# Optimization experiments

Hardware: AMD Instinct MI355X
Metric: run time of the kernel (lower is better)

The kernel has to match this reference:

```python
import jax, jax.numpy as jnp
import numpy as np

V, E, H, DH, C, B, T = 50000, 256, 256, 512, 5, 64, 2048


def setup_inputs() -> dict:
    key = jax.random.key(0)
    ks = jax.random.split(key, 10)
    s = lambda k, sh: (jax.random.normal(k, sh, jnp.float32) * 0.05)
    seqs = jax.random.randint(ks[0], (B, T), 0, V)
    # descending sorted lengths, max length == T (matches max_len = sorted_lens[0])
    lens = jnp.sort(jax.random.randint(ks[1], (B,), T // 4, T + 1))[::-1]
    lens = lens.at[0].set(T).astype(jnp.int32)
    return {
        "seqs": seqs, "lens": lens,
        "emb": s(ks[2], (V, E)),
        "W_ih_f": s(ks[3], (3 * H, E)), "W_hh_f": s(ks[4], (3 * H, H)),
        "b_ih_f": jnp.zeros(3 * H, jnp.float32), "b_hh_f": jnp.zeros(3 * H, jnp.float32),
        "W_ih_b": s(ks[5], (3 * H, E)), "W_hh_b": s(ks[6], (3 * H, H)),
        "b_ih_b": jnp.zeros(3 * H, jnp.float32), "b_hh_b": jnp.zeros(3 * H, jnp.float32),
        "W1": s(ks[7], (DH, 2 * H)), "b1": jnp.zeros(DH, jnp.float32),
        "W2": s(ks[8], (C, DH)), "b2": jnp.zeros(C, jnp.float32),
    }


def _gru_scan(xs, W_ih, W_hh, b_ih, b_hh):
    """xs: [T,B,E]; torch GRUCell semantics, gate order r,z,n. Returns final h [B,H]."""
    gi = jnp.einsum('tbe,ge->tbg', xs, W_ih) + b_ih  # input projections, all steps

    def step(h, gi_t):
        gh = h @ W_hh.T + b_hh
        ir, iz, i_n = jnp.split(gi_t, 3, axis=-1)
        hr, hz, hn = jnp.split(gh, 3, axis=-1)
        r = jax.nn.sigmoid(ir + hr)
        z = jax.nn.sigmoid(iz + hz)
        n = jnp.tanh(i_n + r * hn)
        return (1.0 - z) * n + z * h, None

    h0 = jnp.zeros((xs.shape[1], W_hh.shape[1]), xs.dtype)
    hT, _ = jax.lax.scan(step, h0, gi)
    return hT


def reference(seqs, lens, emb, W_ih_f, W_hh_f, b_ih_f, b_hh_f,
              W_ih_b, W_hh_b, b_ih_b, b_hh_b, W1, b1, W2, b2):
    x = emb[seqs]  # [B,T,E]
    # original LEFT-pads embedded sequences with zeros to max_len
    valid = (jnp.arange(T)[None, :] >= (T - lens)[:, None]).astype(x.dtype)  # [B,T]
    x = x * valid[:, :, None]
    xs = jnp.swapaxes(x, 0, 1)  # [T,B,E]
    hf = _gru_scan(xs, W_ih_f, W_hh_f, b_ih_f, b_hh_f)
    hb = _gru_scan(xs[::-1], W_ih_b, W_hh_b, b_ih_b, b_hh_b)
    rep = jnp.concatenate([hf, hb], axis=1)  # [B,2H]
    h1 = jax.nn.relu(rep @ W1.T + b1)  # dropout is identity in eval
    return jax.nn.softmax(h1 @ W2.T + b2, axis=-1)
```

## Files before the change

### kernel.cpp

```cpp
#include <hip/hip_runtime.h>
#include <stdint.h>

typedef uint32_t u32; typedef uint16_t u16;
typedef __attribute__((ext_vector_type(8))) __bf16 bf16x8;
typedef __attribute__((ext_vector_type(4))) float f32x4;
typedef __attribute__((ext_vector_type(2))) u32 u32x2;
typedef __attribute__((ext_vector_type(4))) u32 u32x4;

#define Vv 50000
#define Ee 256
#define Hh 256
#define Gg 768
#define Bb 64
#define Tt 2048

__device__ __forceinline__ u16 f2bf(float f) {
  u32 x = __builtin_bit_cast(u32, f);
  return (u16)((x + 0x7FFFu + ((x >> 16) & 1u)) >> 16);
}
__device__ __forceinline__ float bf2f(u16 b) {
  u32 x = ((u32)b) << 16;
  return __builtin_bit_cast(float, x);
}
__device__ __forceinline__ u32 pack2(float a, float b) {
  return (u32)f2bf(a) | ((u32)f2bf(b) << 16);
}
__device__ __forceinline__ float sigm(float x) {
  float e = __builtin_amdgcn_exp2f(-1.44269504089f * x);
  return __builtin_amdgcn_rcpf(1.0f + e);
}
__device__ __forceinline__ float tanh_fast(float x) {
  float e = __builtin_amdgcn_exp2f(2.88539008178f * x);
  return 1.0f - 2.0f * __builtin_amdgcn_rcpf(e + 1.0f);
}
__device__ __forceinline__ float bfx(u32x2 v, int q) {
  u32 word = (q & 2) ? v[1] : v[0];
  u16 h = (q & 1) ? (u16)(word >> 16) : (u16)(word & 0xffffu);
  return bf2f(h);
}
__device__ __forceinline__ void block_sync_lds() {
  asm volatile("s_waitcnt lgkmcnt(0)" ::: "memory");
  __builtin_amdgcn_s_barrier();
  asm volatile("" ::: "memory");
}

__global__ void k0_bias(const float* __restrict__ bih_f, const float* __restrict__ bhh_f,
                        const float* __restrict__ bih_b, const float* __restrict__ bhh_b,
                        u16* __restrict__ Pf, u16* __restrict__ Pb) {
  int c = threadIdx.x + blockIdx.x * 256;
  if (c < Gg) {
    float bf_ = bih_f[c] + (c < 512 ? bhh_f[c] : 0.f);
    float bb_ = bih_b[c] + (c < 512 ? bhh_b[c] : 0.f);
    Pf[(size_t)Vv * Gg + c] = f2bf(bf_);
    Pb[(size_t)Vv * Gg + c] = f2bf(bb_);
  }
}

__global__ __launch_bounds__(256) void k1_proj(
    const float* __restrict__ emb, const float* __restrict__ Wih_f,
    const float* __restrict__ Wih_b,
    const float* __restrict__ bih_f, const float* __restrict__ bhh_f,
    const float* __restrict__ bih_b, const float* __restrict__ bhh_b,
    u16* __restrict__ Pf, u16* __restrict__ Pb)
{
  const int t = threadIdx.x, w = t >> 6, l = t & 63;
  const int cl = l & 15, rq = l >> 4;
  const int m0 = blockIdx.x * 128;
  const int dir = blockIdx.y;
  const float* Wih = dir ? Wih_b : Wih_f;
  const float* bih = dir ? bih_b : bih_f;
  const float* bhh = dir ? bhh_b : bhh_f;
  u16* Pd = dir ? Pb : Pf;

  __shared__ __align__(16) u16 As[4096 * 8];
  __shared__ __align__(16) u16 Bs[2048 * 8];

  for (int i = t; i < 4096; i += 256) {
    const int kt = i >> 9, rem = i & 511, row = rem >> 2, rqv = rem & 3;
    const int gm = m0 + row;
    float4 a0 = {0.f,0.f,0.f,0.f}, a1 = {0.f,0.f,0.f,0.f};
    if (gm < Vv) {
      const float* src = emb + (size_t)gm * Ee + kt * 32 + rqv * 8;
      a0 = *(const float4*)src;
      a1 = *(const float4*)(src + 4);
    }
    u32x4 uv = { pack2(a0.x, a0.y), pack2(a0.z, a0.w),
                 pack2(a1.x, a1.y), pack2(a1.z, a1.w) };
    *(u32x4*)(As + (size_t)i * 8) = uv;
  }
  __syncthreads();

  for (int nb = 0; nb < 12; ++nb) {
    for (int i = t; i < 2048; i += 256) {
      const int kt = i >> 8, rem = i & 255, r2 = rem >> 2, rqv = rem & 3;
      const float* src = Wih + (size_t)(nb * 64 + r2) * Ee + kt * 32 + rqv * 8;
      const float4 b0 = *(const float4*)src;
      const float4 b1 = *(const float4*)(src + 4);
      u32x4 uv = { pack2(b0.x, b0.y), pack2(b0.z, b0.w),
                   pack2(b1.x, b1.y), pack2(b1.z, b1.w) };
      *(u32x4*)(Bs + (size_t)i * 8) = uv;
    }
    __syncthreads();

    f32x4 zero4 = {0.f, 0.f, 0.f, 0.f};
    f32x4 acc[2][4];
#pragma unroll
    for (int mt = 0; mt < 2; ++mt)
#pragma unroll
      for (int nt = 0; nt < 4; ++nt) acc[mt][nt] = zero4;

#pragma unroll
    for (int kt = 0; kt < 8; ++kt) {
      bf16x8 af[2], bfr[4];
#pragma unroll
      for (int mt = 0; mt < 2; ++mt)
        af[mt] = *(const bf16x8*)(As + ((size_t)kt * 512 + (w * 32 + mt * 16 + cl) * 4 + rq) * 8);
#pragma unroll
      for (int nt = 0; nt < 4; ++nt)
        bfr[nt] = *(const bf16x8*)(Bs + ((size_t)kt * 256 + (nt * 16 + cl) * 4 + rq) * 8);
#pragma unroll
      for (int mt = 0; mt < 2; ++mt)
#pragma unroll
        for (int nt = 0; nt < 4; ++nt)
          acc[mt][nt] = __builtin_amdgcn_mfma_f32_16x16x32_bf16(af[mt], bfr[nt], acc[mt][nt], 0, 0, 0);
    }

#pragma unroll
    for (int mt = 0; mt < 2; ++mt)
#pragma unroll
      for (int nt = 0; nt < 4; ++nt) {
        const int col = nb * 64 + nt * 16 + cl;
        float bias = bih[col];
        if (col < 512) bias += bhh[col];
#pragma unroll
        for (int q = 0; q < 4; ++q) {
          const int row = m0 + w * 32 + mt * 16 + rq * 4 + q;
          if (row < Vv) Pd[(size_t)row * Gg + col] = f2bf(acc[mt][nt][q] + bias);
        }
      }
    __syncthreads();
  }
}

__global__ __launch_bounds__(512, 2) void k2_rec(
    const int* __restrict__ seqs, const int* __restrict__ lens,
    const float* __restrict__ Whh_f, const float* __restrict__ Whh_b,
    const float* __restrict__ bhh_f, const float* __restrict__ bhh_b,
    const u16* __restrict__ Pf, const u16* __restrict__ Pb,
    float* __restrict__ rep)
{
  const int tid = threadIdx.x, w = tid >> 6, l = tid & 63;
  const int cl = l & 15, rq = l >> 4;
  const int dir = (int)blockIdx.x >> 2;
  const int b0 = ((int)blockIdx.x & 3) * 16;

  const float* Whh = dir ? Whh_b : Whh_f;
  const float* bhh = dir ? bhh_b : bhh_f;
  const u16* P = dir ? Pb : Pf;

  __shared__ __align__(16) u16 h_lds[8192];

  bf16x8 wfrag[3][2][8];
#pragma unroll
  for (int g = 0; g < 3; ++g)
#pragma unroll
    for (int bi = 0; bi < 2; ++bi) {
      const int c = g * 256 + (2 * w + bi) * 16 + cl;
      const float* wr = Whh + (size_t)c * Hh;
#pragma unroll
      for (int kb = 0; kb < 8; ++kb) {
        const int k0 = kb * 32 + rq * 8;
        const float4 f0 = *(const float4*)(wr + k0);
        const float4 f1 = *(const float4*)(wr + k0 + 4);
        u32x4 uv = { pack2(f0.x, f0.y), pack2(f0.z, f0.w),
                     pack2(f1.x, f1.y), pack2(f1.z, f1.w) };
        wfrag[g][bi][kb] = __builtin_bit_cast(bf16x8, uv);
      }
    }

  const float* bhhn0 = bhh + 512 + w * 32 + rq * 4;
  const float* bhhn1 = bhhn0 + 16;

  float hprev[2][4];
#pragma unroll
  for (int bi = 0; bi < 2; ++bi)
#pragma unroll
    for (int q = 0; q < 4; ++q) hprev[bi][q] = 0.f;

  const int myrow = b0 + cl;
  const int mylen = lens[myrow];
  const int* myseq = seqs + (size_t)myrow * Tt;
  const int vthr = Tt - mylen;

  for (int i = tid; i < 4096; i += 512) ((u32*)h_lds)[i] = 0;

  const int xk = (cl >> 1);
  const int rdoff = cl * 64 + (((rq + xk) & 3) << 4);
  const int wr0 = w * 1024 + cl * 64 + ((((rq >> 1) + xk) & 3) << 4) + (rq & 1) * 8;
  const int wr1 = w * 1024 + cl * 64 + ((((rq >> 1) + 2 + xk) & 3) << 4) + (rq & 1) * 8;

  const int colb0 = w * 32 + rq * 4;

  u32x2 gi0[3], gi1[3];
  {
    const int tk = myseq[dir ? (Tt - 1) : 0];
    const int valid = dir ? (0 < mylen) : (0 >= vthr);
    const u32 off = (valid ? (u32)tk : (u32)Vv) * (u32)(Gg * 2);
    const u16* pr = (const u16*)((const char*)P + off) + colb0;
#pragma unroll
    for (int g = 0; g < 3; ++g) {
      gi0[g] = *(const u32x2*)(pr + g * 256);
      gi1[g] = *(const u32x2*)(pr + g * 256 + 16);
    }
  }
  int tok1 = myseq[dir ? (Tt - 2) : 1];
  block_sync_lds();

  int bb = 0;
#pragma unroll 1
  for (int s = 0; s < Tt; ++s) {
    const char* hb = (const char*)h_lds + bb;
    char* hn = (char*)h_lds + (bb ^ 8192);

    f32x4 zero4 = {0.f, 0.f, 0.f, 0.f};
    f32x4 ar0 = zero4, az0 = zero4, ar1 = zero4, az1 = zero4;
    f32x4 an0 = *(const f32x4*)bhhn0;
    f32x4 an1 = *(const f32x4*)bhhn1;

#pragma unroll
    for (int kb = 0; kb < 8; ++kb) {
      const bf16x8 hf = *(const bf16x8*)(hb + kb * 1024 + rdoff);
      ar0 = __builtin_amdgcn_mfma_f32_16x16x32_bf16(wfrag[0][0][kb], hf, ar0, 0, 0, 0);
      az0 = __builtin_amdgcn_mfma_f32_16x16x32_bf16(wfrag[1][0][kb], hf, az0, 0, 0, 0);
      an0 = __builtin_amdgcn_mfma_f32_16x16x32_bf16(wfrag[2][0][kb], hf, an0, 0, 0, 0);
      ar1 = __builtin_amdgcn_mfma_f32_16x16x32_bf16(wfrag[0][1][kb], hf, ar1, 0, 0, 0);
      az1 = __builtin_amdgcn_mfma_f32_16x16x32_bf16(wfrag[1][1][kb], hf, az1, 0, 0, 0);
      an1 = __builtin_amdgcn_mfma_f32_16x16x32_bf16(wfrag[2][1][kb], hf, an1, 0, 0, 0);
    }

    int tok2 = tok1;
    if (s + 2 < Tt) tok2 = myseq[dir ? (Tt - 3 - s) : (s + 2)];

    const int validn = dir ? (s + 1 < mylen) : (s + 1 >= vthr);
    const u32 offn = (validn ? (u32)tok1 : (u32)Vv) * (u32)(Gg * 2);
    const u16* prn = (const u16*)((const char*)P + offn) + colb0;

#define GATES(BI, GIS, AR, AZ, AN, WRO, PRADD)                                   \
    {                                                                            \
      float hq[4];                                                               \
      _Pragma("unroll")                                                          \
      for (int q = 0; q < 4; ++q) {                                              \
        const float ir = bfx(GIS[0], q);                                         \
        const float iz = bfx(GIS[1], q);                                         \
        const float in_ = bfx(GIS[2], q);                                        \
        const float r = sigm(ir + AR[q]);                                        \
        const float z = sigm(iz + AZ[q]);                                        \
        const float n = tanh_fast(fmaf(r, AN[q], in_));                          \
        const float hv = fmaf(z, hprev[BI][q] - n, n);                           \
        hprev[BI][q] = hv;                                                       \
        hq[q] = hv;                                                              \
      }                                                                          \
      u32 p0, p1;                                                                \
      asm("v_cvt_pk_bf16_f32 %0, %1, %2" : "=v"(p0) : "v"(hq[0]), "v"(hq[1]));   \
      asm("v_cvt_pk_bf16_f32 %0, %1, %2" : "=v"(p1) : "v"(hq[2]), "v"(hq[3]));   \
      u32x2 hw = {p0, p1};                                                       \
      *(u32x2*)(hn + (bb ^ 8192) * 0 + WRO) = hw;                                \
      _Pragma("unroll")                                                          \
      for (int g = 0; g < 3; ++g) GIS[g] = *(const u32x2*)(prn + g * 256 + PRADD); \
    }

    GATES(0, gi0, ar0, az0, an0, wr0, 0)
    GATES(1, gi1, ar1, az1, an1, wr1, 16)
#undef GATES

    tok1 = tok2;
    bb ^= 8192;
    block_sync_lds();
  }

#pragma unroll
  for (int bi = 0; bi < 2; ++bi)
#pragma unroll
    for (int q = 0; q < 4; ++q) {
      const int col = w * 32 + bi * 16 + rq * 4 + q;
      rep[(size_t)(b0 + cl) * (2 * Hh) + dir * Hh + col] = hprev[bi][q];
    }
}

__global__ __launch_bounds__(256) void k3a(
    const float* __restrict__ rep, const float* __restrict__ W1,
    const float* __restrict__ b1, float* __restrict__ h1)
{
  __shared__ float rl[512];
  const int b = blockIdx.x, t = threadIdx.x;
  rl[t] = rep[(size_t)b * 512 + t];
  rl[t + 256] = rep[(size_t)b * 512 + 256 + t];
  __syncthreads();
#pragma unroll
  for (int oo = 0; oo < 2; ++oo) {
    const int o = t + oo * 256;
    const float4* wr = (const float4*)(W1 + (size_t)o * 512);
    const float4* rr = (const float4*)rl;
    float acc = 0.f;
#pragma unroll 8
    for (int k = 0; k < 128; ++k) {
      const float4 wv = wr[k], rv = rr[k];
      acc += wv.x * rv.x + wv.y * rv.y + wv.z * rv.z + wv.w * rv.w;
    }
    h1[(size_t)b * 512 + o] = fmaxf(acc + b1[o], 0.f);
  }
}

__global__ __launch_bounds__(320) void k3b(
    const float* __restrict__ h1, const float* __restrict__ W2,
    const float* __restrict__ b2, float* __restrict__ out)
{
  __shared__ float lg[64 * 5];
  const int t = threadIdx.x;
  const int c = t >> 6, b = t & 63;
  const float4* hr = (const float4*)(h1 + (size_t)b * 512);
  const float4* wr = (const float4*)(W2 + (size_t)c * 512);
  float acc = 0.f;
#pragma unroll 8
  for (int k = 0; k < 128; ++k) {
    const float4 hv = hr[k], wv = wr[k];
    acc += hv.x * wv.x + hv.y * wv.y + hv.z * wv.z + hv.w * wv.w;
  }
  lg[b * 5 + c] = acc + b2[c];
  __syncthreads();
  if (t < 64) {
    float v[5];
#pragma unroll
    for (int i = 0; i < 5; ++i) v[i] = lg[t * 5 + i];
    float m = v[0];
#pragma unroll
    for (int i = 1; i < 5; ++i) m = fmaxf(m, v[i]);
    float ssum = 0.f;
#pragma unroll
    for (int i = 0; i < 5; ++i) {
      v[i] = __builtin_amdgcn_exp2f(1.44269504089f * (v[i] - m));
      ssum += v[i];
    }
    const float inv = 1.0f / ssum;
#pragma unroll
    for (int i = 0; i < 5; ++i) out[t * 5 + i] = v[i] * inv;
  }
}

extern "C" void kernel_launch(void* const* d_in, const int* in_sizes, int n_in,
                              void* d_out, int out_size, void* d_ws, size_t ws_size,
                              hipStream_t stream) {
  const int* seqs = (const int*)d_in[0];
  const int* lens = (const int*)d_in[1];
  const float* emb = (const float*)d_in[2];
  const float* Wih_f = (const float*)d_in[3];
  const float* Whh_f = (const float*)d_in[4];
  const float* bih_f = (const float*)d_in[5];
  const float* bhh_f = (const float*)d_in[6];
  const float* Wih_b = (const float*)d_in[7];
  const float* Whh_b = (const float*)d_in[8];
  const float* bih_b = (const float*)d_in[9];
  const float* bhh_b = (const float*)d_in[10];
  const float* W1 = (const float*)d_in[11];
  const float* b1 = (const float*)d_in[12];
  const float* W2 = (const float*)d_in[13];
  const float* b2 = (const float*)d_in[14];
  float* out = (float*)d_out;

  char* ws = (char*)d_ws;
  const size_t PSZ = (size_t)(Vv + 1) * Gg * 2;
  u16* Pf = (u16*)ws;
  u16* Pb = (u16*)(ws + PSZ);
  float* rep = (float*)(ws + 2 * PSZ);
  float* h1 = (float*)(ws + 2 * PSZ + 131072);

  hipLaunchKernelGGL(k0_bias, dim3(3), dim3(256), 0, stream,
                     bih_f, bhh_f, bih_b, bhh_b, Pf, Pb);
  hipLaunchKernelGGL(k1_proj, dim3(391, 2), dim3(256), 0, stream,
                     emb, Wih_f, Wih_b, bih_f, bhh_f, bih_b, bhh_b, Pf, Pb);
  hipLaunchKernelGGL(k2_rec, dim3(8), dim3(512), 0, stream,
                     seqs, lens, Whh_f, Whh_b, bhh_f, bhh_b, Pf, Pb, rep);
  hipLaunchKernelGGL(k3a, dim3(64), dim3(256), 0, stream, rep, W1, b1, h1);
  hipLaunchKernelGGL(k3b, dim3(1), dim3(320), 0, stream, h1, W2, b2, out);
}
```

Before: 6.093 ms.

## Split projection GEMM over N blocks and tune recurrent kernel scheduling

The vocabulary projection kernel now launches four times as many blocks, each handling three of the twelve output column tiles. This spreads the 50k-row table projection across more CUs, at the cost of reconverting the embedding tile in every block. The recurrent kernel hoists the n-gate bias into registers, raises wave priority around the MFMA loop, and replaces the custom waitcnt+barrier with __syncthreads. It also simplifies bf16 unpacking, removes the unroll-1 pragma, and changes launch bounds to waves_per_eu. Together these target the projection kernel's low occupancy and per-step overhead in the sequential loop.

```diff
diff --git a/kernel.cpp b/kernel.cpp
--- a/kernel.cpp
+++ b/kernel.cpp
@@ -18,10 +18,6 @@
   u32 x = __builtin_bit_cast(u32, f);
   return (u16)((x + 0x7FFFu + ((x >> 16) & 1u)) >> 16);
 }
-__device__ __forceinline__ float bf2f(u16 b) {
-  u32 x = ((u32)b) << 16;
-  return __builtin_bit_cast(float, x);
-}
 __device__ __forceinline__ u32 pack2(float a, float b) {
   return (u32)f2bf(a) | ((u32)f2bf(b) << 16);
 }
@@ -33,16 +29,8 @@
   float e = __builtin_amdgcn_exp2f(2.88539008178f * x);
   return 1.0f - 2.0f * __builtin_amdgcn_rcpf(e + 1.0f);
 }
-__device__ __forceinline__ float bfx(u32x2 v, int q) {
-  u32 word = (q & 2) ? v[1] : v[0];
-  u16 h = (q & 1) ? (u16)(word >> 16) : (u16)(word & 0xffffu);
-  return bf2f(h);
-}
-__device__ __forceinline__ void block_sync_lds() {
-  asm volatile("s_waitcnt lgkmcnt(0)" ::: "memory");
-  __builtin_amdgcn_s_barrier();
-  asm volatile("" ::: "memory");
-}
+__device__ __forceinline__ float bflo(u32 v) { return __builtin_bit_cast(float, v << 16); }
+__device__ __forceinline__ float bfhi(u32 v) { return __builtin_bit_cast(float, v & 0xffff0000u); }
 
 __global__ void k0_bias(const float* __restrict__ bih_f, const float* __restrict__ bhh_f,
                         const float* __restrict__ bih_b, const float* __restrict__ bhh_b,
@@ -67,6 +55,7 @@
   const int cl = l & 15, rq = l >> 4;
   const int m0 = blockIdx.x * 128;
   const int dir = blockIdx.y;
+  const int nbase = blockIdx.z * 3;
   const float* Wih = dir ? Wih_b : Wih_f;
   const float* bih = dir ? bih_b : bih_f;
   const float* bhh = dir ? bhh_b : bhh_f;
@@ -90,7 +79,8 @@
   }
   __syncthreads();
 
-  for (int nb = 0; nb < 12; ++nb) {
+  for (int nbo = 0; nbo < 3; ++nbo) {
+    const int nb = nbase + nbo;
     for (int i = t; i < 2048; i += 256) {
       const int kt = i >> 8, rem = i & 255, r2 = rem >> 2, rqv = rem & 3;
       const float* src = Wih + (size_t)(nb * 64 + r2) * Ee + kt * 32 + rqv * 8;
@@ -142,7 +132,8 @@
   }
 }
 
-__global__ __launch_bounds__(512, 2) void k2_rec(
+__global__ __launch_bounds__(512, 1) __attribute__((amdgpu_waves_per_eu(2)))
+void k2_rec(
     const int* __restrict__ seqs, const int* __restrict__ lens,
     const float* __restrict__ Whh_f, const float* __restrict__ Whh_b,
     const float* __restrict__ bhh_f, const float* __restrict__ bhh_b,
@@ -178,8 +169,8 @@
       }
     }
 
-  const float* bhhn0 = bhh + 512 + w * 32 + rq * 4;
-  const float* bhhn1 = bhhn0 + 16;
+  f32x4 bhn0 = *(const f32x4*)(bhh + 512 + w * 32 + rq * 4);
+  f32x4 bhn1 = *(const f32x4*)(bhh + 512 + w * 32 + 16 + rq * 4);
 
   float hprev[2][4];
 #pragma unroll
@@ -214,19 +205,18 @@
     }
   }
   int tok1 = myseq[dir ? (Tt - 2) : 1];
-  block_sync_lds();
+  __syncthreads();
 
   int bb = 0;
-#pragma unroll 1
   for (int s = 0; s < Tt; ++s) {
     const char* hb = (const char*)h_lds + bb;
     char* hn = (char*)h_lds + (bb ^ 8192);
 
     f32x4 zero4 = {0.f, 0.f, 0.f, 0.f};
     f32x4 ar0 = zero4, az0 = zero4, ar1 = zero4, az1 = zero4;
-    f32x4 an0 = *(const f32x4*)bhhn0;
-    f32x4 an1 = *(const f32x4*)bhhn1;
-
+    f32x4 an0 = bhn0;
+    f32x4 an1 = bhn1;
+    __builtin_amdgcn_s_setprio(1);
 #pragma unroll
     for (int kb = 0; kb < 8; ++kb) {
       const bf16x8 hf = *(const bf16x8*)(hb + kb * 1024 + rdoff);
@@ -237,6 +227,7 @@
       az1 = __builtin_amdgcn_mfma_f32_16x16x32_bf16(wfrag[1][1][kb], hf, az1, 0, 0, 0);
       an1 = __builtin_amdgcn_mfma_f32_16x16x32_bf16(wfrag[2][1][kb], hf, an1, 0, 0, 0);
     }
+    __builtin_amdgcn_s_setprio(0);
 
     int tok2 = tok1;
     if (s + 2 < Tt) tok2 = myseq[dir ? (Tt - 3 - s) : (s + 2)];
@@ -250,9 +241,12 @@
       float hq[4];                                                               \
       _Pragma("unroll")                                                          \
       for (int q = 0; q < 4; ++q) {                                              \
-        const float ir = bfx(GIS[0], q);                                         \
-        const float iz = bfx(GIS[1], q);                                         \
-        const float in_ = bfx(GIS[2], q);                                        \
+        const u32 wr_ = (q & 2) ? GIS[0][1] : GIS[0][0];                         \
+        const u32 wz_ = (q & 2) ? GIS[1][1] : GIS[1][0];                         \
+        const u32 wn_ = (q & 2) ? GIS[2][1] : GIS[2][0];                         \
+        const float ir = (q & 1) ? bfhi(wr_) : bflo(wr_);                        \
+        const float iz = (q & 1) ? bfhi(wz_) : bflo(wz_);                        \
+        const float in_ = (q & 1) ? bfhi(wn_) : bflo(wn_);                       \
         const float r = sigm(ir + AR[q]);                                        \
         const float z = sigm(iz + AZ[q]);                                        \
         const float n = tanh_fast(fmaf(r, AN[q], in_));                          \
@@ -264,7 +258,7 @@
       asm("v_cvt_pk_bf16_f32 %0, %1, %2" : "=v"(p0) : "v"(hq[0]), "v"(hq[1]));   \
       asm("v_cvt_pk_bf16_f32 %0, %1, %2" : "=v"(p1) : "v"(hq[2]), "v"(hq[3]));   \
       u32x2 hw = {p0, p1};                                                       \
-      *(u32x2*)(hn + (bb ^ 8192) * 0 + WRO) = hw;                                \
+      *(u32x2*)(hn + WRO) = hw;                                                  \
       _Pragma("unroll")                                                          \
       for (int g = 0; g < 3; ++g) GIS[g] = *(const u32x2*)(prn + g * 256 + PRADD); \
     }
@@ -275,7 +269,7 @@
 
     tok1 = tok2;
     bb ^= 8192;
-    block_sync_lds();
+    __syncthreads();
   }
 
 #pragma unroll
@@ -376,7 +370,7 @@
 
   hipLaunchKernelGGL(k0_bias, dim3(3), dim3(256), 0, stream,
                      bih_f, bhh_f, bih_b, bhh_b, Pf, Pb);
-  hipLaunchKernelGGL(k1_proj, dim3(391, 2), dim3(256), 0, stream,
+  hipLaunchKernelGGL(k1_proj, dim3(391, 2, 4), dim3(256), 0, stream,
                      emb, Wih_f, Wih_b, bih_f, bhh_f, bih_b, bhh_b, Pf, Pb);
   hipLaunchKernelGGL(k2_rec, dim3(8), dim3(512), 0, stream,
                      seqs, lens, Whh_f, Whh_b, bhh_f, bhh_b, Pf, Pb, rep);
```

After: 6.467 ms. +6.2%, slower.
